# Performance work log

Measured on AMD Instinct MI355X. Metric: run time of the kernel, lower is better.

The kernel has to match this reference:

```python
import jax, jax.numpy as jnp
import numpy as np

N_NODES = 100000
N_EDGES = 1600000
IN_DIM = 128
HID_DIM = 128
OUT_DIM = 2


def sage_conv(x, src, dst, deg_inv, W_l, W_r, b):
    # mean-aggregate neighbor features: messages flow src -> dst
    agg = jax.ops.segment_sum(x[src], dst, num_segments=N_NODES)  # [N, d_in]
    agg = agg * deg_inv[:, None]
    # PyG SAGEConv: out = lin_l(aggr) + lin_r(x); bias only on lin_l
    return agg @ W_l + x @ W_r + b


def setup_inputs() -> dict:
    key = jax.random.key(0)
    ks = jax.random.split(key, 9)
    x = jax.random.normal(ks[0], (N_NODES, IN_DIM), dtype=jnp.float32)
    edge_index = jax.random.randint(ks[1], (2, N_EDGES), 0, N_NODES, dtype=jnp.int64)

    def glorot(k, shape):
        lim = float(np.sqrt(6.0 / (shape[0] + shape[1])))
        return jax.random.uniform(k, shape, jnp.float32, -lim, lim)

    return {
        "x": x,
        "edge_index": edge_index,
        "W1_l": glorot(ks[2], (IN_DIM, HID_DIM)),
        "W1_r": glorot(ks[3], (IN_DIM, HID_DIM)),
        "b1": jnp.zeros((HID_DIM,), jnp.float32),
        "W2_l": glorot(ks[4], (HID_DIM, HID_DIM)),
        "W2_r": glorot(ks[5], (HID_DIM, HID_DIM)),
        "b2": jnp.zeros((HID_DIM,), jnp.float32),
        "W3_l": glorot(ks[6], (HID_DIM, OUT_DIM)),
        "W3_r": glorot(ks[7], (HID_DIM, OUT_DIM)),
        "b3": jnp.zeros((OUT_DIM,), jnp.float32),
    }


def reference(x, edge_index, W1_l, W1_r, b1, W2_l, W2_r, b2, W3_l, W3_r, b3):
    src, dst = edge_index[0], edge_index[1]
    # mean-aggregation normalization: 1/in-degree (clamped to >=1)
    deg = jax.ops.segment_sum(jnp.ones((N_EDGES,), jnp.float32), dst, num_segments=N_NODES)
    deg_inv = 1.0 / jnp.maximum(deg, 1.0)

    h = sage_conv(x, src, dst, deg_inv, W1_l, W1_r, b1)
    h = jax.nn.relu(h)  # dropout is identity in eval mode
    h = sage_conv(h, src, dst, deg_inv, W2_l, W2_r, b2)
    h = jax.nn.relu(h)
    h = sage_conv(h, src, dst, deg_inv, W3_l, W3_r, b3)
    h = jax.nn.relu(h)
    return jax.nn.log_softmax(h, axis=1)
```

## Files before the change

### kernel.cpp

```cpp
#include <hip/hip_runtime.h>
#include <math.h>

#define DIM 128

typedef __attribute__((ext_vector_type(8))) short bf16x8;
typedef __attribute__((ext_vector_type(4))) float f32x4;

__device__ __forceinline__ ushort f2bf(float f) {
  unsigned u = __float_as_uint(f);
  return (ushort)((u + 0x7FFFu + ((u >> 16) & 1u)) >> 16);
}
__device__ __forceinline__ float bf2f(ushort h) {
  return __uint_as_float(((unsigned)h) << 16);
}


__global__ __launch_bounds__(256) void count_cast_kernel(
    const int* __restrict__ dst, unsigned* __restrict__ counts, int E, int NB, int NBUCK,
    const float* __restrict__ x, ushort* __restrict__ xh, long total_f,
    const float* __restrict__ W1l, const float* __restrict__ W1r,
    const float* __restrict__ W2l, const float* __restrict__ W2r,
    ushort* __restrict__ tabs, int CB) {
  __shared__ unsigned hist[1024];
  const int tid = threadIdx.x;
  int bid = blockIdx.x;
  if (bid < NB) {
    for (int i = tid; i < NBUCK; i += 256) hist[i] = 0u;
    __syncthreads();
    long base = (long)bid * 2048;
#pragma unroll
    for (int c = 0; c < 8; ++c) {
      long e = base + c * 256 + tid;
      if (e < E) atomicAdd(&hist[((unsigned)dst[e]) >> 7], 1u);
    }
    __syncthreads();
    for (int i = tid; i < NBUCK; i += 256)
      counts[(size_t)bid * NBUCK + i] = hist[i];
    return;
  }
  int aid = bid - NB;
  if (aid < CB) {
    long i = ((long)aid * 2048 + tid) * 4;
    for (int c = 0; c < 8; ++c, i += 1024) {
      if (i >= total_f) break;
      float4 v = *(const float4*)(x + i);
      uint2 Hh;
      Hh.x = (unsigned)f2bf(v.x) | ((unsigned)f2bf(v.y) << 16);
      Hh.y = (unsigned)f2bf(v.z) | ((unsigned)f2bf(v.w) << 16);
      *(uint2*)(xh + i) = Hh;
    }
    return;
  }
  int aid2 = aid - CB;
  if (aid2 < 256) {
    int m = aid2 >> 6;
    const float* W = (m == 0) ? W1l : (m == 1) ? W1r : (m == 2) ? W2l : W2r;
    ushort* Ht = tabs + (size_t)m * 16384;
    int idx = (aid2 & 63) * 256 + tid;
    int k = idx >> 7, n = idx & 127;
    Ht[n * DIM + k] = f2bf(W[idx]);
  }
}

__global__ __launch_bounds__(256) void colscan_kernel(unsigned* __restrict__ counts,
                                                      unsigned* __restrict__ totals,
                                                      int NB, int NBUCK) {
  int wid = (blockIdx.x << 2) + (threadIdx.x >> 6);
  int lane = threadIdx.x & 63;
  if (wid >= NBUCK) return;
  unsigned carry = 0u;
  for (int k0 = 0; k0 < NB; k0 += 64) {
    int k = k0 + lane;
    unsigned v = (k < NB) ? counts[(size_t)k * NBUCK + wid] : 0u;
    unsigned s = v;
#pragma unroll
    for (int o = 1; o < 64; o <<= 1) {
      unsigned t = __shfl_up(s, o, 64);
      if (lane >= o) s += t;
    }
    if (k < NB) counts[(size_t)k * NBUCK + wid] = carry + s - v;
    carry += __shfl(s, 63, 64);
  }
  if (lane == 0) totals[wid] = carry;
}

__global__ __launch_bounds__(256) void totscan_kernel(unsigned* __restrict__ totals,
                                                      int NBUCK, int E) {
  __shared__ unsigned s[256];
  __shared__ unsigned carry;
  if (threadIdx.x == 0) carry = 0u;
  __syncthreads();
  for (int base = 0; base < NBUCK; base += 256) {
    int i = base + threadIdx.x;
    unsigned v = (i < NBUCK) ? totals[i] : 0u;
    s[threadIdx.x] = v;
    __syncthreads();
#pragma unroll
    for (int d = 1; d < 256; d <<= 1) {
      unsigned t = (threadIdx.x >= d) ? s[threadIdx.x - d] : 0u;
      __syncthreads();
      s[threadIdx.x] += t;
      __syncthreads();
    }
    if (i < NBUCK) totals[i] = carry + s[threadIdx.x] - v;
    __syncthreads();
    if (threadIdx.x == 0) carry += s[255];
    __syncthreads();
  }
  if (threadIdx.x == 0) totals[NBUCK] = (unsigned)E;
}

__global__ __launch_bounds__(256) void cscatter_kernel(
    const int* __restrict__ src, const int* __restrict__ dst,
    const unsigned* __restrict__ counts, const unsigned* __restrict__ totals,
    unsigned* __restrict__ pairs, int E, int NBUCK) {
  __shared__ unsigned basec[1024];
  const int tid = threadIdx.x;
  const int bid = blockIdx.x;
  for (int i = tid; i < NBUCK; i += 256)
    basec[i] = counts[(size_t)bid * NBUCK + i] + totals[i];
  __syncthreads();
  long base = (long)bid * 2048;
#pragma unroll
  for (int c = 0; c < 8; ++c) {
    long e = base + c * 256 + tid;
    if (e < E) {
      unsigned d = (unsigned)dst[e];
      unsigned pos = atomicAdd(&basec[d >> 7], 1u);
      pairs[pos] = ((unsigned)src[e] << 7) | (d & 127u);
    }
  }
}

__global__ __launch_bounds__(256) void fine_kernel(
    const unsigned* __restrict__ pairs, const unsigned* __restrict__ totals,
    int* __restrict__ csr_src, unsigned* __restrict__ offs, float* __restrict__ dinv,
    int N, int NBUCK, int E) {
  __shared__ int lsrc[4096];
  __shared__ ushort ldst[4096];
  __shared__ unsigned hist[128], excl[128], cur[128];
  const int tid = threadIdx.x;
  const int b = blockIdx.x;
  const unsigned t0 = totals[b], t1 = totals[b + 1];
  unsigned cnt = t1 - t0;
  if (cnt > 4096u) cnt = 4096u;
  if (tid < 128) { hist[tid] = 0u; cur[tid] = 0u; }
  __syncthreads();
  for (unsigned i = tid; i < cnt; i += 256) {
    unsigned p = pairs[t0 + i];
    lsrc[i] = (int)(p >> 7);
    int nl = (int)(p & 127u);
    ldst[i] = (ushort)nl;
    atomicAdd(&hist[nl], 1u);
  }
  __syncthreads();
  if (tid < 64) {
    unsigned v0 = hist[tid], v1 = hist[tid + 64];
    unsigned s0 = v0, s1 = v1;
#pragma unroll
    for (int o = 1; o < 64; o <<= 1) {
      unsigned u0 = __shfl_up(s0, o, 64);
      unsigned u1 = __shfl_up(s1, o, 64);
      if (tid >= o) { s0 += u0; s1 += u1; }
    }
    unsigned tot0 = __shfl(s0, 63, 64);
    excl[tid] = s0 - v0;
    excl[tid + 64] = tot0 + s1 - v1;
  }
  __syncthreads();
  if (tid < 128) {
    int node = (b << 7) + tid;
    if (node < N) {
      offs[node] = t0 + excl[tid];
      dinv[node] = 1.0f / fmaxf((float)hist[tid], 1.0f);
    }
  }
  if (b == 0 && tid == 255) offs[N] = (unsigned)E;
  for (unsigned i = tid; i < cnt; i += 256) {
    int nl = (int)ldst[i];
    unsigned slot = excl[nl] + atomicAdd(&cur[nl], 1u);
    csr_src[t0 + slot] = lsrc[i];
  }
}


#define GATHER_BODY(TABLE)                                                       \
  const int node = (blockIdx.x * 256 + threadIdx.x) >> 6;                        \
  if (node >= N) return;                                                         \
  const int lane = threadIdx.x & 63;                                             \
  const int eslot = lane >> 4;                                                   \
  const int col = lane & 15;                                                     \
  const unsigned beg = off[node], end = off[node + 1];                           \
  const ushort* fbase = (TABLE) + col * 8;                                       \
  float acc[8];                                                                  \
  _Pragma("unroll") for (int t = 0; t < 8; ++t) acc[t] = 0.f;                    \
  auto accum = [&](int4 v) {                                                     \
    unsigned w0 = (unsigned)v.x, w1 = (unsigned)v.y;                             \
    unsigned w2 = (unsigned)v.z, w3 = (unsigned)v.w;                             \
    acc[0] += __uint_as_float(w0 << 16);                                         \
    acc[1] += __uint_as_float(w0 & 0xFFFF0000u);                                 \
    acc[2] += __uint_as_float(w1 << 16);                                         \
    acc[3] += __uint_as_float(w1 & 0xFFFF0000u);                                 \
    acc[4] += __uint_as_float(w2 << 16);                                         \
    acc[5] += __uint_as_float(w2 & 0xFFFF0000u);                                 \
    acc[6] += __uint_as_float(w3 << 16);                                         \
    acc[7] += __uint_as_float(w3 & 0xFFFF0000u);                                 \
  };                                                                             \
  unsigned base = beg;                                                           \
  for (; base + 16 <= end; base += 16) {                                         \
    int s0 = csr_src[base + eslot];                                              \
    int s1 = csr_src[base + 4 + eslot];                                          \
    int s2 = csr_src[base + 8 + eslot];                                          \
    int s3 = csr_src[base + 12 + eslot];                                         \
    int4 v0 = *(const int4*)(fbase + (size_t)s0 * DIM);                          \
    int4 v1 = *(const int4*)(fbase + (size_t)s1 * DIM);                          \
    int4 v2 = *(const int4*)(fbase + (size_t)s2 * DIM);                          \
    int4 v3 = *(const int4*)(fbase + (size_t)s3 * DIM);                          \
    accum(v0); accum(v1); accum(v2); accum(v3);                                  \
  }                                                                              \
  if (base < end) {                                                              \
    unsigned e0 = base + eslot, e1 = base + 4 + eslot;                           \
    unsigned e2 = base + 8 + eslot, e3 = base + 12 + eslot;                      \
    int s0 = csr_src[e0 < end ? e0 : end - 1];                                   \
    int s1 = csr_src[e1 < end ? e1 : end - 1];                                   \
    int s2 = csr_src[e2 < end ? e2 : end - 1];                                   \
    int s3 = csr_src[e3 < end ? e3 : end - 1];                                   \
    int4 v0 = *(const int4*)(fbase + (size_t)s0 * DIM);                          \
    int4 v1 = *(const int4*)(fbase + (size_t)s1 * DIM);                          \
    int4 v2 = *(const int4*)(fbase + (size_t)s2 * DIM);                          \
    int4 v3 = *(const int4*)(fbase + (size_t)s3 * DIM);                          \
    if (e0 < end) accum(v0);                                                     \
    if (e1 < end) accum(v1);                                                     \
    if (e2 < end) accum(v2);                                                     \
    if (e3 < end) accum(v3);                                                     \
  }                                                                              \
  _Pragma("unroll") for (int t = 0; t < 8; ++t) {                                \
    acc[t] += __shfl_xor(acc[t], 32, 64);                                        \
    acc[t] += __shfl_xor(acc[t], 16, 64);                                        \
  }

__global__ __launch_bounds__(256) void gather_wave_kernel(
    const ushort* __restrict__ featH, const int* __restrict__ csr_src,
    const unsigned* __restrict__ off, const float* __restrict__ dinv,
    ushort* __restrict__ aggH, int N) {
  GATHER_BODY(featH)
  if (eslot == 0) {
    float di = dinv[node];
    unsigned ph[4];
#pragma unroll
    for (int t = 0; t < 4; ++t) {
      ph[t] = (unsigned)f2bf(acc[2 * t] * di) | ((unsigned)f2bf(acc[2 * t + 1] * di) << 16);
    }
    *(int4*)(aggH + (size_t)node * DIM + col * 8) =
        make_int4((int)ph[0], (int)ph[1], (int)ph[2], (int)ph[3]);
  }
}

__global__ __launch_bounds__(256) void gather2_kernel(
    const ushort* __restrict__ h1l, const int* __restrict__ csr_src,
    const unsigned* __restrict__ off, const float* __restrict__ dinv,
    const ushort* __restrict__ h1r, const float* __restrict__ W3l,
    const float* __restrict__ W3r, float* __restrict__ y, int N) {
  GATHER_BODY(h1l)
  if (eslot == 0) {
    float di = dinv[node];
    int4 xv = *(const int4*)(h1r + (size_t)node * DIM + col * 8);
    unsigned w0 = (unsigned)xv.x, w1 = (unsigned)xv.y;
    unsigned w2 = (unsigned)xv.z, w3 = (unsigned)xv.w;
    float h[8];
    h[0] = fmaxf(acc[0] * di + __uint_as_float(w0 << 16), 0.f);
    h[1] = fmaxf(acc[1] * di + __uint_as_float(w0 & 0xFFFF0000u), 0.f);
    h[2] = fmaxf(acc[2] * di + __uint_as_float(w1 << 16), 0.f);
    h[3] = fmaxf(acc[3] * di + __uint_as_float(w1 & 0xFFFF0000u), 0.f);
    h[4] = fmaxf(acc[4] * di + __uint_as_float(w2 << 16), 0.f);
    h[5] = fmaxf(acc[5] * di + __uint_as_float(w2 & 0xFFFF0000u), 0.f);
    h[6] = fmaxf(acc[6] * di + __uint_as_float(w3 << 16), 0.f);
    h[7] = fmaxf(acc[7] * di + __uint_as_float(w3 & 0xFFFF0000u), 0.f);
    const int d0 = col * 8;
    float y0 = 0.f, y1 = 0.f, y2 = 0.f, y3 = 0.f;
#pragma unroll
    for (int t = 0; t < 8; t += 2) {
      float4 wl = *(const float4*)(W3l + (size_t)(d0 + t) * 2);
      float4 wr = *(const float4*)(W3r + (size_t)(d0 + t) * 2);
      y0 += h[t] * wl.x + h[t + 1] * wl.z;
      y1 += h[t] * wl.y + h[t + 1] * wl.w;
      y2 += h[t] * wr.x + h[t + 1] * wr.z;
      y3 += h[t] * wr.y + h[t + 1] * wr.w;
    }
#pragma unroll
    for (int o = 1; o < 16; o <<= 1) {
      y0 += __shfl_xor(y0, o, 64);
      y1 += __shfl_xor(y1, o, 64);
      y2 += __shfl_xor(y2, o, 64);
      y3 += __shfl_xor(y3, o, 64);
    }
    if (lane == 0) *(float4*)(y + (size_t)node * 4) = make_float4(y0, y1, y2, y3);
  }
}

__global__ __launch_bounds__(256) void sage_mfma_kernel(
    const ushort* __restrict__ aggH, const ushort* xH,
    const ushort* __restrict__ WlH, const ushort* __restrict__ WrH,
    const float* __restrict__ bias, ushort* __restrict__ outH, int N) {
  __shared__ ushort As[128 * 64];
  __shared__ ushort Bs[128 * 64];

  const int tid = threadIdx.x;
  const int bm = blockIdx.x * 128;
  const int wave = tid >> 6;
  const int lane = tid & 63;
  const int l15 = lane & 15;
  const int quad = lane >> 4;
  const int wm = wave >> 1;
  const int wn = wave & 1;

  f32x4 acc[4][4];
#pragma unroll
  for (int i = 0; i < 4; ++i)
#pragma unroll
    for (int j = 0; j < 4; ++j) acc[i][j] = (f32x4){0.f, 0.f, 0.f, 0.f};

  for (int g = 0; g < 4; ++g) {
    const ushort* Ap = (g < 2) ? aggH : xH;
    const ushort* Wp = (g < 2) ? WlH : WrH;
    const int kt = (g & 1) << 6;
    __syncthreads();
#pragma unroll
    for (int c = 0; c < 4; ++c) {
      int flat = c * 256 + tid;
      int row = flat >> 3;
      int kg = flat & 7;
      int swz = (kg ^ (row & 7)) << 3;
      int grow = bm + row;
      if (grow >= N) grow = N - 1;
      *(int4*)(&As[row * 64 + swz]) = *(const int4*)(Ap + (size_t)grow * DIM + kt + kg * 8);
      *(int4*)(&Bs[row * 64 + swz]) = *(const int4*)(Wp + (size_t)row * DIM + kt + kg * 8);
    }
    __syncthreads();
#pragma unroll
    for (int ks = 0; ks < 2; ++ks) {
      bf16x8 af[4], bfr[4];
      int kg = (ks << 2) + quad;
#pragma unroll
      for (int i = 0; i < 4; ++i) {
        int ar = (wm << 6) + (i << 4) + l15;
        af[i] = *(const bf16x8*)(&As[ar * 64 + ((kg ^ (ar & 7)) << 3)]);
        int br = (wn << 6) + (i << 4) + l15;
        bfr[i] = *(const bf16x8*)(&Bs[br * 64 + ((kg ^ (br & 7)) << 3)]);
      }
#pragma unroll
      for (int i = 0; i < 4; ++i)
#pragma unroll
        for (int j = 0; j < 4; ++j)
          acc[i][j] = __builtin_amdgcn_mfma_f32_16x16x32_bf16(af[i], bfr[j], acc[i][j], 0, 0, 0);
    }
  }

  float bv[4];
#pragma unroll
  for (int j = 0; j < 4; ++j) bv[j] = bias[(wn << 6) + (j << 4) + l15];

  __syncthreads();
#pragma unroll
  for (int i = 0; i < 4; ++i)
#pragma unroll
    for (int j = 0; j < 4; ++j)
#pragma unroll
      for (int r = 0; r < 4; ++r) {
        int row = (wm << 6) + (i << 4) + (quad << 2) + r;
        int colc = (wn << 6) + (j << 4) + l15;
        ((ushort*)As)[((row & 63) << 7) + colc + ((row >> 6) << 13)] =
            f2bf(fmaxf(acc[i][j][r] + bv[j], 0.f));
      }
  __syncthreads();
#pragma unroll
  for (int c = 0; c < 8; ++c) {
    int flat = c * 256 + tid;
    int row = flat >> 4;
    int grow = bm + row;
    if (grow < N)
      *(int4*)(outH + (size_t)grow * DIM + (flat & 15) * 8) =
          *(const int4*)((const ushort*)As + flat * 8);
  }
}

__global__ __launch_bounds__(256) void gemm2_dual_kernel(
    const ushort* __restrict__ h1, const ushort* __restrict__ tabs2,
    const float* __restrict__ b2, ushort* __restrict__ h1l, ushort* __restrict__ h1r, int N) {
  __shared__ ushort L[3 * 128 * 64];
  ushort* As = L;
  ushort* Bs0 = L + 8192;
  ushort* Bs1 = L + 16384;
  const int tid = threadIdx.x;
  const int bm = blockIdx.x * 128;
  const int wave = tid >> 6;
  const int lane = tid & 63;
  const int l15 = lane & 15;
  const int quad = lane >> 4;
  const int wm = wave >> 1;
  const int wn = wave & 1;

  f32x4 accl[4][4], accr[4][4];
#pragma unroll
  for (int i = 0; i < 4; ++i)
#pragma unroll
    for (int j = 0; j < 4; ++j) {
      accl[i][j] = (f32x4){0.f, 0.f, 0.f, 0.f};
      accr[i][j] = (f32x4){0.f, 0.f, 0.f, 0.f};
    }

  for (int g = 0; g < 2; ++g) {
    const int kt = g << 6;
    __syncthreads();
#pragma unroll
    for (int c = 0; c < 4; ++c) {
      int flat = c * 256 + tid;
      int row = flat >> 3;
      int kg = flat & 7;
      int swz = (kg ^ (row & 7)) << 3;
      int grow = bm + row;
      if (grow >= N) grow = N - 1;
      *(int4*)(&As[row * 64 + swz]) = *(const int4*)(h1 + (size_t)grow * DIM + kt + kg * 8);
      *(int4*)(&Bs0[row * 64 + swz]) = *(const int4*)(tabs2 + (size_t)row * DIM + kt + kg * 8);
      *(int4*)(&Bs1[row * 64 + swz]) =
          *(const int4*)(tabs2 + 16384 + (size_t)row * DIM + kt + kg * 8);
    }
    __syncthreads();
#pragma unroll
    for (int ks = 0; ks < 2; ++ks) {
      bf16x8 af[4], bl[4], br[4];
      int kg = (ks << 2) + quad;
#pragma unroll
      for (int i = 0; i < 4; ++i) {
        int ar = (wm << 6) + (i << 4) + l15;
        af[i] = *(const bf16x8*)(&As[ar * 64 + ((kg ^ (ar & 7)) << 3)]);
        int nr = (wn << 6) + (i << 4) + l15;
        bl[i] = *(const bf16x8*)(&Bs0[nr * 64 + ((kg ^ (nr & 7)) << 3)]);
        br[i] = *(const bf16x8*)(&Bs1[nr * 64 + ((kg ^ (nr & 7)) << 3)]);
      }
#pragma unroll
      for (int i = 0; i < 4; ++i)
#pragma unroll
        for (int j = 0; j < 4; ++j) {
          accl[i][j] = __builtin_amdgcn_mfma_f32_16x16x32_bf16(af[i], bl[j], accl[i][j], 0, 0, 0);
          accr[i][j] = __builtin_amdgcn_mfma_f32_16x16x32_bf16(af[i], br[j], accr[i][j], 0, 0, 0);
        }
    }
  }

  float bv[4];
#pragma unroll
  for (int j = 0; j < 4; ++j) bv[j] = b2[(wn << 6) + (j << 4) + l15];

#pragma unroll
  for (int m = 0; m < 2; ++m) {
    __syncthreads();
#pragma unroll
    for (int i = 0; i < 4; ++i)
#pragma unroll
      for (int j = 0; j < 4; ++j)
#pragma unroll
        for (int r = 0; r < 4; ++r) {
          int row = (wm << 6) + (i << 4) + (quad << 2) + r;
          int colc = (wn << 6) + (j << 4) + l15;
          float v = m ? (accr[i][j][r] + bv[j]) : accl[i][j][r];
          L[row * 128 + colc] = f2bf(v);
        }
    __syncthreads();
    ushort* out = m ? h1r : h1l;
#pragma unroll
    for (int c = 0; c < 8; ++c) {
      int flat = c * 256 + tid;
      int row = flat >> 4;
      int grow = bm + row;
      if (grow < N)
        *(int4*)(out + (size_t)grow * DIM + (flat & 15) * 8) = *(const int4*)(&L[flat * 8]);
    }
  }
}

__global__ __launch_bounds__(256) void final3_kernel(const float* __restrict__ y,
                                                     const int* __restrict__ csr_src,
                                                     const unsigned* __restrict__ off,
                                                     const float* __restrict__ dinv,
                                                     const float* __restrict__ b3,
                                                     float* __restrict__ out, int N) {
  int n = blockIdx.x * 256 + threadIdx.x;
  if (n >= N) return;
  unsigned beg = off[n], end = off[n + 1];
  float s0 = 0.f, s1 = 0.f;
  for (unsigned e = beg; e < end; ++e) {
    int s = csr_src[e];
    float2 v = *reinterpret_cast<const float2*>(&y[(size_t)s * 4]);
    s0 += v.x; s1 += v.y;
  }
  float di = dinv[n];
  float o0 = fmaxf(s0 * di + y[(size_t)n * 4 + 2] + b3[0], 0.f);
  float o1 = fmaxf(s1 * di + y[(size_t)n * 4 + 3] + b3[1], 0.f);
  float m = fmaxf(o0, o1);
  float l = m + logf(expf(o0 - m) + expf(o1 - m));
  out[n * 2 + 0] = o0 - l;
  out[n * 2 + 1] = o1 - l;
}

extern "C" void kernel_launch(void* const* d_in, const int* in_sizes, int n_in,
                              void* d_out, int out_size, void* d_ws, size_t ws_size,
                              hipStream_t stream) {
  const float* x   = (const float*)d_in[0];
  const int*   ei  = (const int*)d_in[1];
  const float* W1l = (const float*)d_in[2];
  const float* W1r = (const float*)d_in[3];
  const float* b1  = (const float*)d_in[4];
  const float* W2l = (const float*)d_in[5];
  const float* W2r = (const float*)d_in[6];
  const float* b2  = (const float*)d_in[7];
  const float* W3l = (const float*)d_in[8];
  const float* W3r = (const float*)d_in[9];
  const float* b3  = (const float*)d_in[10];

  const int N = in_sizes[0] / DIM;
  const int E = in_sizes[1] / 2;
  const int* src = ei;
  const int* dst = ei + E;

  const int NBUCK = (N + 127) >> 7;
  const int NB    = (E + 2047) / 2048;
  const long total_f = (long)N * DIM;
  const int CB    = (int)((total_f / 4 + 2047) / 2048);

  char* ws = (char*)d_ws;
  size_t off_b = 0;
  auto alloc = [&](size_t bytes) {
    void* p = ws + off_b;
    off_b = (off_b + bytes + 255) & ~(size_t)255;
    return p;
  };
  unsigned* counts  = (unsigned*)alloc((size_t)NB * NBUCK * 4);
  unsigned* totals  = (unsigned*)alloc((size_t)(NBUCK + 1) * 4);
  void*     shared_ = alloc((size_t)N * DIM * 2);
  unsigned* pairs   = (unsigned*)shared_;
  ushort*   aggH    = (ushort*)shared_;
  ushort*   h1l     = (ushort*)shared_;
  int*      csr_src = (int*)alloc((size_t)E * 4);
  unsigned* offs    = (unsigned*)alloc((size_t)(N + 1) * 4);
  float*    dinv    = (float*)alloc((size_t)N * 4);
  ushort*   xh      = (ushort*)alloc((size_t)N * DIM * 2);
  ushort*   tabs    = (ushort*)alloc((size_t)4 * 16384 * 2);
  float*    y       = (float*)alloc((size_t)N * 4 * 4);
  ushort*   h1r     = (ushort*)alloc((size_t)N * DIM * 2);

  count_cast_kernel<<<NB + CB + 256, 256, 0, stream>>>(
      dst, counts, E, NB, NBUCK, x, xh, total_f, W1l, W1r, W2l, W2r, tabs, CB);
  colscan_kernel<<<(NBUCK + 3) / 4, 256, 0, stream>>>(counts, totals, NB, NBUCK);
  totscan_kernel<<<1, 256, 0, stream>>>(totals, NBUCK, E);
  cscatter_kernel<<<NB, 256, 0, stream>>>(src, dst, counts, totals, pairs, E, NBUCK);
  fine_kernel<<<NBUCK, 256, 0, stream>>>(pairs, totals, csr_src, offs, dinv, N, NBUCK, E);

  const ushort* W1lH = tabs;
  const ushort* W1rH = tabs + 16384;
  const ushort* tabs2 = tabs + 32768;
  const int G = (N + 127) / 128;
  const int gather_grid = (N + 3) / 4;

  gather_wave_kernel<<<gather_grid, 256, 0, stream>>>(xh, csr_src, offs, dinv, aggH, N);
  sage_mfma_kernel<<<G, 256, 0, stream>>>(aggH, xh, W1lH, W1rH, b1, xh, N);
  gemm2_dual_kernel<<<G, 256, 0, stream>>>(xh, tabs2, b2, h1l, h1r, N);
  gather2_kernel<<<gather_grid, 256, 0, stream>>>(h1l, csr_src, offs, dinv, h1r, W3l, W3r, y, N);
  final3_kernel<<<(N + 255) / 256, 256, 0, stream>>>(y, csr_src, offs, dinv, b3, (float*)d_out, N);
}
```

Before: 353.7 us.

## Fuse layer-1 SAGE GEMM with layer-2 dual GEMM, keep h1 in LDS

The layer-1 MFMA kernel and the layer-2 dual-projection GEMM become one kernel. The relu'd layer-1 output tile stays in shared memory in swizzled layout and is used directly as the A operand for the second GEMM, which removes the h1 global write and reread and one launch. B fragments for layer 2 now come straight from global memory (tabs2) instead of through LDS. The gather2 epilogue now spreads the per-node layer-3 projection across all four edge slots with a wider shuffle reduction instead of running it only in slot 0. Reading B from global on every k-step may add latency and cache traffic, and LDS use drops, which could change occupancy.

Measured after the change: 368.7 us. 1.04x slower.

```diff
diff --git a/kernel.cpp b/kernel.cpp
--- a/kernel.cpp
+++ b/kernel.cpp
@@ -262,33 +262,22 @@
     const ushort* __restrict__ h1r, const float* __restrict__ W3l,
     const float* __restrict__ W3r, float* __restrict__ y, int N) {
   GATHER_BODY(h1l)
-  if (eslot == 0) {
+  {
     float di = dinv[node];
-    int4 xv = *(const int4*)(h1r + (size_t)node * DIM + col * 8);
-    unsigned w0 = (unsigned)xv.x, w1 = (unsigned)xv.y;
-    unsigned w2 = (unsigned)xv.z, w3 = (unsigned)xv.w;
-    float h[8];
-    h[0] = fmaxf(acc[0] * di + __uint_as_float(w0 << 16), 0.f);
-    h[1] = fmaxf(acc[1] * di + __uint_as_float(w0 & 0xFFFF0000u), 0.f);
-    h[2] = fmaxf(acc[2] * di + __uint_as_float(w1 << 16), 0.f);
-    h[3] = fmaxf(acc[3] * di + __uint_as_float(w1 & 0xFFFF0000u), 0.f);
-    h[4] = fmaxf(acc[4] * di + __uint_as_float(w2 << 16), 0.f);
-    h[5] = fmaxf(acc[5] * di + __uint_as_float(w2 & 0xFFFF0000u), 0.f);
-    h[6] = fmaxf(acc[6] * di + __uint_as_float(w3 << 16), 0.f);
-    h[7] = fmaxf(acc[7] * di + __uint_as_float(w3 & 0xFFFF0000u), 0.f);
-    const int d0 = col * 8;
-    float y0 = 0.f, y1 = 0.f, y2 = 0.f, y3 = 0.f;
-#pragma unroll
-    for (int t = 0; t < 8; t += 2) {
-      float4 wl = *(const float4*)(W3l + (size_t)(d0 + t) * 2);
-      float4 wr = *(const float4*)(W3r + (size_t)(d0 + t) * 2);
-      y0 += h[t] * wl.x + h[t + 1] * wl.z;
-      y1 += h[t] * wl.y + h[t + 1] * wl.w;
-      y2 += h[t] * wr.x + h[t + 1] * wr.z;
-      y3 += h[t] * wr.y + h[t + 1] * wr.w;
-    }
-#pragma unroll
-    for (int o = 1; o < 16; o <<= 1) {
+    float a0 = (eslot == 0) ? acc[0] : (eslot == 1) ? acc[2] : (eslot == 2) ? acc[4] : acc[6];
+    float a1 = (eslot == 0) ? acc[1] : (eslot == 1) ? acc[3] : (eslot == 2) ? acc[5] : acc[7];
+    const int d0 = col * 8 + eslot * 2;
+    unsigned hv = *(const unsigned*)(h1r + (size_t)node * DIM + d0);
+    float h0 = fmaxf(a0 * di + __uint_as_float(hv << 16), 0.f);
+    float h1v = fmaxf(a1 * di + __uint_as_float(hv & 0xFFFF0000u), 0.f);
+    float4 wl = *(const float4*)(W3l + (size_t)d0 * 2);
+    float4 wr = *(const float4*)(W3r + (size_t)d0 * 2);
+    float y0 = h0 * wl.x + h1v * wl.z;
+    float y1 = h0 * wl.y + h1v * wl.w;
+    float y2 = h0 * wr.x + h1v * wr.z;
+    float y3 = h0 * wr.y + h1v * wr.w;
+#pragma unroll
+    for (int o = 1; o < 64; o <<= 1) {
       y0 += __shfl_xor(y0, o, 64);
       y1 += __shfl_xor(y1, o, 64);
       y2 += __shfl_xor(y2, o, 64);
@@ -298,12 +287,15 @@
   }
 }
 
-__global__ __launch_bounds__(256) void sage_mfma_kernel(
-    const ushort* __restrict__ aggH, const ushort* xH,
+__global__ __launch_bounds__(256) void sage_fused_kernel(
+    const ushort* __restrict__ aggH, const ushort* __restrict__ xH,
     const ushort* __restrict__ WlH, const ushort* __restrict__ WrH,
-    const float* __restrict__ bias, ushort* __restrict__ outH, int N) {
-  __shared__ ushort As[128 * 64];
-  __shared__ ushort Bs[128 * 64];
+    const float* __restrict__ b1, const ushort* __restrict__ tabs2,
+    const float* __restrict__ b2,
+    ushort* __restrict__ h1l, ushort* __restrict__ h1r, int N) {
+  __shared__ ushort L[2 * 128 * 64];
+  ushort* As = L;
+  ushort* Bs = L + 8192;
 
   const int tid = threadIdx.x;
   const int bm = blockIdx.x * 128;
@@ -356,9 +348,9 @@
     }
   }
 
-  float bv[4];
-#pragma unroll
-  for (int j = 0; j < 4; ++j) bv[j] = bias[(wn << 6) + (j << 4) + l15];
+  float bv1[4];
+#pragma unroll
+  for (int j = 0; j < 4; ++j) bv1[j] = b1[(wn << 6) + (j << 4) + l15];
 
   __syncthreads();
 #pragma unroll
@@ -369,36 +361,12 @@
       for (int r = 0; r < 4; ++r) {
         int row = (wm << 6) + (i << 4) + (quad << 2) + r;
         int colc = (wn << 6) + (j << 4) + l15;
-        ((ushort*)As)[((row & 63) << 7) + colc + ((row >> 6) << 13)] =
-            f2bf(fmaxf(acc[i][j][r] + bv[j], 0.f));
+        ushort* Hbuf = (colc & 64) ? Bs : As;
+        int kin = colc & 63;
+        Hbuf[row * 64 + ((((kin >> 3) ^ (row & 7))) << 3) + (kin & 7)] =
+            f2bf(fmaxf(acc[i][j][r] + bv1[j], 0.f));
       }
   __syncthreads();
-#pragma unroll
-  for (int c = 0; c < 8; ++c) {
-    int flat = c * 256 + tid;
-    int row = flat >> 4;
-    int grow = bm + row;
-    if (grow < N)
-      *(int4*)(outH + (size_t)grow * DIM + (flat & 15) * 8) =
-          *(const int4*)((const ushort*)As + flat * 8);
-  }
-}
-
-__global__ __launch_bounds__(256) void gemm2_dual_kernel(
-    const ushort* __restrict__ h1, const ushort* __restrict__ tabs2,
-    const float* __restrict__ b2, ushort* __restrict__ h1l, ushort* __restrict__ h1r, int N) {
-  __shared__ ushort L[3 * 128 * 64];
-  ushort* As = L;
-  ushort* Bs0 = L + 8192;
-  ushort* Bs1 = L + 16384;
-  const int tid = threadIdx.x;
-  const int bm = blockIdx.x * 128;
-  const int wave = tid >> 6;
-  const int lane = tid & 63;
-  const int l15 = lane & 15;
-  const int quad = lane >> 4;
-  const int wm = wave >> 1;
-  const int wn = wave & 1;
 
   f32x4 accl[4][4], accr[4][4];
 #pragma unroll
@@ -409,48 +377,36 @@
       accr[i][j] = (f32x4){0.f, 0.f, 0.f, 0.f};
     }
 
-  for (int g = 0; g < 2; ++g) {
-    const int kt = g << 6;
-    __syncthreads();
-#pragma unroll
-    for (int c = 0; c < 4; ++c) {
-      int flat = c * 256 + tid;
-      int row = flat >> 3;
-      int kg = flat & 7;
-      int swz = (kg ^ (row & 7)) << 3;
-      int grow = bm + row;
-      if (grow >= N) grow = N - 1;
-      *(int4*)(&As[row * 64 + swz]) = *(const int4*)(h1 + (size_t)grow * DIM + kt + kg * 8);
-      *(int4*)(&Bs0[row * 64 + swz]) = *(const int4*)(tabs2 + (size_t)row * DIM + kt + kg * 8);
-      *(int4*)(&Bs1[row * 64 + swz]) =
-          *(const int4*)(tabs2 + 16384 + (size_t)row * DIM + kt + kg * 8);
-    }
-    __syncthreads();
+#pragma unroll
+  for (int g2 = 0; g2 < 2; ++g2) {
+    const int kt = g2 << 6;
+    const ushort* Hbuf = g2 ? Bs : As;
 #pragma unroll
     for (int ks = 0; ks < 2; ++ks) {
-      bf16x8 af[4], bl[4], br[4];
       int kg = (ks << 2) + quad;
+      bf16x8 af[4];
 #pragma unroll
       for (int i = 0; i < 4; ++i) {
         int ar = (wm << 6) + (i << 4) + l15;
-        af[i] = *(const bf16x8*)(&As[ar * 64 + ((kg ^ (ar & 7)) << 3)]);
-        int nr = (wn << 6) + (i << 4) + l15;
-        bl[i] = *(const bf16x8*)(&Bs0[nr * 64 + ((kg ^ (nr & 7)) << 3)]);
-        br[i] = *(const bf16x8*)(&Bs1[nr * 64 + ((kg ^ (nr & 7)) << 3)]);
+        af[i] = *(const bf16x8*)(&Hbuf[ar * 64 + ((kg ^ (ar & 7)) << 3)]);
       }
 #pragma unroll
-      for (int i = 0; i < 4; ++i)
-#pragma unroll
-        for (int j = 0; j < 4; ++j) {
-          accl[i][j] = __builtin_amdgcn_mfma_f32_16x16x32_bf16(af[i], bl[j], accl[i][j], 0, 0, 0);
-          accr[i][j] = __builtin_amdgcn_mfma_f32_16x16x32_bf16(af[i], br[j], accr[i][j], 0, 0, 0);
+      for (int j = 0; j < 4; ++j) {
+        int nr = (wn << 6) + (j << 4) + l15;
+        bf16x8 bl = *(const bf16x8*)(tabs2 + (size_t)nr * DIM + kt + kg * 8);
+        bf16x8 br = *(const bf16x8*)(tabs2 + 16384 + (size_t)nr * DIM + kt + kg * 8);
+#pragma unroll
+        for (int i = 0; i < 4; ++i) {
+          accl[i][j] = __builtin_amdgcn_mfma_f32_16x16x32_bf16(af[i], bl, accl[i][j], 0, 0, 0);
+          accr[i][j] = __builtin_amdgcn_mfma_f32_16x16x32_bf16(af[i], br, accr[i][j], 0, 0, 0);
         }
-    }
-  }
-
-  float bv[4];
-#pragma unroll
-  for (int j = 0; j < 4; ++j) bv[j] = b2[(wn << 6) + (j << 4) + l15];
+      }
+    }
+  }
+
+  float bv2[4];
+#pragma unroll
+  for (int j = 0; j < 4; ++j) bv2[j] = b2[(wn << 6) + (j << 4) + l15];
 
 #pragma unroll
   for (int m = 0; m < 2; ++m) {
@@ -463,7 +419,7 @@
         for (int r = 0; r < 4; ++r) {
           int row = (wm << 6) + (i << 4) + (quad << 2) + r;
           int colc = (wn << 6) + (j << 4) + l15;
-          float v = m ? (accr[i][j][r] + bv[j]) : accl[i][j][r];
+          float v = m ? (accr[i][j][r] + bv2[j]) : accl[i][j][r];
           L[row * 128 + colc] = f2bf(v);
         }
     __syncthreads();
@@ -563,8 +519,7 @@
   const int gather_grid = (N + 3) / 4;
 
   gather_wave_kernel<<<gather_grid, 256, 0, stream>>>(xh, csr_src, offs, dinv, aggH, N);
-  sage_mfma_kernel<<<G, 256, 0, stream>>>(aggH, xh, W1lH, W1rH, b1, xh, N);
-  gemm2_dual_kernel<<<G, 256, 0, stream>>>(xh, tabs2, b2, h1l, h1r, N);
+  sage_fused_kernel<<<G, 256, 0, stream>>>(aggH, xh, W1lH, W1rH, b1, tabs2, b2, h1l, h1r, N);
   gather2_kernel<<<gather_grid, 256, 0, stream>>>(h1l, csr_src, offs, dinv, h1r, W3l, W3r, y, N);
   final3_kernel<<<(N + 255) / 256, 256, 0, stream>>>(y, csr_src, offs, dinv, b3, (float*)d_out, N);
 }
```
